# Kernel tuning notes

Measured on AMD Instinct MI355X. Metric: run time of the kernel, lower is better.

Reference implementation:

```python
import jax, jax.numpy as jnp
import numpy as np

E = 1024
H = 16          # num_heads
D = E // H      # head_dim
HID = 1024      # hidden_dim
B, S = 16, 512
EPS = 1e-5


def _ln(x, g, b):
    mu = jnp.mean(x, axis=-1, keepdims=True)
    var = jnp.mean(jnp.square(x - mu), axis=-1, keepdims=True)
    return (x - mu) * jax.lax.rsqrt(var + EPS) * g + b


def setup_inputs() -> dict:
    key = jax.random.key(0)
    ks = jax.random.split(key, 8)
    s = 1.0 / np.sqrt(E)
    return {
        'state_features': jax.random.normal(ks[0], (6, B, S, E), jnp.float32),
        'Wq': jax.random.normal(ks[1], (E, E), jnp.float32) * s,
        'bq': jnp.zeros((E,), jnp.float32),
        'Wk': jax.random.normal(ks[2], (E, E), jnp.float32) * s,
        'bk': jnp.zeros((E,), jnp.float32),
        'Wv': jax.random.normal(ks[3], (E, E), jnp.float32) * s,
        'bv': jnp.zeros((E,), jnp.float32),
        'Wo': jax.random.normal(ks[4], (E, E), jnp.float32) * s,
        'bo': jnp.zeros((E,), jnp.float32),
        'ln1_g': jnp.ones((E,), jnp.float32),
        'ln1_b': jnp.zeros((E,), jnp.float32),
        'fusion_w': jnp.ones((6,), jnp.float32) / 6.0,
        'Wf': jax.random.normal(ks[5], (HID, E), jnp.float32) * s,
        'bf': jnp.zeros((HID,), jnp.float32),
        'ln2_g': jnp.ones((HID,), jnp.float32),
        'ln2_b': jnp.zeros((HID,), jnp.float32),
    }


def reference(state_features, Wq, bq, Wk, bk, Wv, bv, Wo, bo,
              ln1_g, ln1_b, fusion_w, Wf, bf, ln2_g, ln2_b):
    # state_features: (6, B, S, E) -> stacked (N, 6, E), N = B*S
    st = jnp.transpose(state_features, (1, 2, 0, 3)).reshape(B * S, 6, E)
    N = st.shape[0]

    q = (st @ Wq.T + bq).reshape(N, 6, H, D)
    k = (st @ Wk.T + bk).reshape(N, 6, H, D)
    v = (st @ Wv.T + bv).reshape(N, 6, H, D)

    # tiny 6x6 attention per token per head (dropout = identity in eval)
    scores = jnp.einsum('nqhd,nkhd->nhqk', q, k) / np.sqrt(D).astype(np.float32)
    attn = jax.nn.softmax(scores, axis=-1)
    ctx = jnp.einsum('nhqk,nkhd->nqhd', attn, v).reshape(N, 6, E)

    out = ctx @ Wo.T + bo
    enhanced = _ln(out + st, ln1_g, ln1_b)  # (N, 6, E)

    # weighted_sum fusion
    w = jax.nn.softmax(fusion_w)
    fused = jnp.einsum('nse,s->ne', enhanced, w)

    hidden = fused @ Wf.T + bf
    hidden = jnp.where(hidden >= 0, hidden, 0.01 * hidden)  # LeakyReLU(0.01)
    hidden = _ln(hidden, ln2_g, ln2_b)
    return hidden.reshape(B, S, HID)
```

## Files before the change

### kernel.cpp

```cpp
#include <hip/hip_runtime.h>
#include <hip/hip_bf16.h>

#define NTOK 8192
#define E 1024
#define NS 6
#define MBIG (NTOK * NS)
#define NSE ((long)NTOK * E)

typedef short short8 __attribute__((ext_vector_type(8)));
typedef float f32x4 __attribute__((ext_vector_type(4)));
typedef unsigned short ushort4v __attribute__((ext_vector_type(4)));

#define TM 128
#define TN 128
#define BK 64

static __device__ __forceinline__ float bf2f(unsigned short u) {
    union { unsigned int i; float f; } c; c.i = ((unsigned int)u) << 16; return c.f;
}

struct WPtrs { const float* s[5]; __hip_bfloat16* d[5]; };
__global__ __launch_bounds__(256) void cvt5_w(WPtrs p)
{
    const int seg = blockIdx.x >> 10;
    const int i = ((blockIdx.x & 1023) * 256 + threadIdx.x) * 4;
    const float4 v = *(const float4*)(p.s[seg] + i);
    union { __hip_bfloat16 h[4]; unsigned long long u; } pk;
    pk.h[0] = (__hip_bfloat16)v.x;
    pk.h[1] = (__hip_bfloat16)v.y;
    pk.h[2] = (__hip_bfloat16)v.z;
    pk.h[3] = (__hip_bfloat16)v.w;
    *(unsigned long long*)(p.d[seg] + i) = pk.u;
}

__global__ __launch_bounds__(256) void cvt_bulk(
    const float* __restrict__ src, __hip_bfloat16* __restrict__ dst)
{
    const long i = ((long)blockIdx.x * 256 + threadIdx.x) * 4;
    const float4 v = *(const float4*)(src + i);
    union { __hip_bfloat16 h[4]; unsigned long long u; } pk;
    pk.h[0] = (__hip_bfloat16)v.x;
    pk.h[1] = (__hip_bfloat16)v.y;
    pk.h[2] = (__hip_bfloat16)v.z;
    pk.h[3] = (__hip_bfloat16)v.w;
    *(unsigned long long*)(dst + i) = pk.u;
}

#define NITER  8

struct GOut { __hip_bfloat16* C[3]; const float* bias[3]; };

static __device__ __forceinline__ void stage_half(
    const __hip_bfloat16* gsrc,
    __hip_bfloat16* ldst, int tid)
{
#pragma unroll
    for (int piece = 0; piece < 2; ++piece) {
        const int r  = piece * 64 + (tid >> 3);
        const int s  = tid & 7;
        const int ss = s ^ (r & 7);
        const __hip_bfloat16* g = gsrc + (long)r * 1024 + ss * 8;
        __hip_bfloat16* l = ldst + r * 64 + s * 8;
        __builtin_amdgcn_global_load_lds((const __attribute__((address_space(1))) void*)g,
                                         (__attribute__((address_space(3))) void*)l, 16, 0, 0);
    }
}

static __device__ __forceinline__ short8 ld_frag(
    const __hip_bfloat16* half_base, int lr, int slot)
{
    return *(const short8*)(half_base + lr * 64 + ((slot ^ (lr & 7)) << 3));
}

#define STAGE(kt, part)                                                         \
  {                                                                             \
    const int _b  = (kt) & 1;                                                   \
    const int _ab = (part) >> 1;                                                \
    const int _hf = (part) & 1;                                                 \
    const __hip_bfloat16* _g = (_ab == 0)                                       \
        ? A  + (m0 + _hf * 128) * 1024 + (kt) * 64                              \
        : Wb + ((long)n0 + _hf * 128) * 1024 + (kt) * 64;                       \
    stage_half(_g, &lds[((_b * 2 + _ab) * 2 + _hf) * 8192], tid);               \
  }

#define PH(kt, q, HASNEXT, nkt, STMT_STAGE, STMT_WAIT)                          \
  {                                                                             \
    STMT_STAGE;                                                                 \
    STMT_WAIT;                                                                  \
    __builtin_amdgcn_s_barrier();                                               \
    asm volatile("s_waitcnt lgkmcnt(0)" ::: "memory");                          \
    __builtin_amdgcn_sched_barrier(0);                                          \
    __builtin_amdgcn_s_setprio(1);                                              \
    _Pragma("unroll") for (int mf = 0; mf < 2; ++mf)                            \
      _Pragma("unroll") for (int nf = 0; nf < 4; ++nf)                          \
        _Pragma("unroll") for (int k2 = 0; k2 < 2; ++k2)                        \
          acc[(q) * 2 + mf][nf] = __builtin_amdgcn_mfma_f32_16x16x32_bf16(      \
              bfr[nf][k2], afr[(q) & 1][mf][k2], acc[(q) * 2 + mf][nf], 0,0,0); \
    __builtin_amdgcn_s_setprio(0);                                              \
    if ((q) < 3) {                                                              \
      const __hip_bfloat16* _Ab = &lds[((((kt) & 1) * 2 + 0) * 2 + wm) * 8192]; \
      _Pragma("unroll") for (int mf = 0; mf < 2; ++mf)                          \
        _Pragma("unroll") for (int k2 = 0; k2 < 2; ++k2)                        \
          afr[((q) + 1) & 1][mf][k2] =                                          \
              ld_frag(_Ab, ((q) + 1) * 32 + mf * 16 + mrow, k2 * 4 + quad);     \
    } else if (HASNEXT) {                                                       \
      const __hip_bfloat16* _An = &lds[((((nkt) & 1) * 2 + 0) * 2 + wm) * 8192];\
      const __hip_bfloat16* _Bn =                                               \
          &lds[((((nkt) & 1) * 2 + 1) * 2 + (wn >> 1)) * 8192];                 \
      _Pragma("unroll") for (int nf = 0; nf < 4; ++nf)                          \
        _Pragma("unroll") for (int k2 = 0; k2 < 2; ++k2)                        \
          bfr[nf][k2] = ld_frag(_Bn, (wn & 1) * 64 + nf * 16 + mrow,            \
                                k2 * 4 + quad);                                 \
      _Pragma("unroll") for (int mf = 0; mf < 2; ++mf)                          \
        _Pragma("unroll") for (int k2 = 0; k2 < 2; ++k2)                        \
          afr[0][mf][k2] = ld_frag(_An, mf * 16 + mrow, k2 * 4 + quad);         \
    }                                                                           \
    __builtin_amdgcn_s_barrier();                                               \
  }

__global__ __launch_bounds__(512) void gemm256(
    const __hip_bfloat16* __restrict__ A,
    const __hip_bfloat16* __restrict__ Wb,
    GOut out)
{
    __shared__ __hip_bfloat16 lds[2 * 2 * 2 * 8192] __attribute__((aligned(16)));

    const int tid  = threadIdx.x;
    const int lane = tid & 63;
    const int wid  = tid >> 6;
    const int quad = lane >> 4;
    const int mrow = lane & 15;
    const int wm = wid >> 2;
    const int wn = wid & 3;

    const int gx  = gridDim.x;
    const int nwg = gx * gridDim.y;
    const int cpx = nwg >> 3;
    const int lin = blockIdx.y * gx + blockIdx.x;
    const int tile = (lin & 7) * cpx + (lin >> 3);
    const int  n0 = (tile % gx) * 256;
    const long m0 = (long)(tile / gx) * 256;

    f32x4 acc[8][4] = {};
    short8 bfr[4][2];
    short8 afr[2][2][2];

    STAGE(0, 0); STAGE(0, 1); STAGE(0, 2); STAGE(0, 3);
    STAGE(1, 2); STAGE(1, 3);
    asm volatile("s_waitcnt vmcnt(4)" ::: "memory");
    __builtin_amdgcn_s_barrier();

    {
        const __hip_bfloat16* _Ab = &lds[(0 * 2 + wm) * 8192];
        const __hip_bfloat16* _Bb = &lds[((0 * 2 + 1) * 2 + (wn >> 1)) * 8192];
#pragma unroll
        for (int nf = 0; nf < 4; ++nf)
#pragma unroll
            for (int k2 = 0; k2 < 2; ++k2)
                bfr[nf][k2] = ld_frag(_Bb, (wn & 1) * 64 + nf * 16 + mrow, k2 * 4 + quad);
#pragma unroll
        for (int mf = 0; mf < 2; ++mf)
#pragma unroll
            for (int k2 = 0; k2 < 2; ++k2)
                afr[0][mf][k2] = ld_frag(_Ab, mf * 16 + mrow, k2 * 4 + quad);
    }

#pragma unroll 1
    for (int it = 0; it < NITER; ++it) {
        const int kt0 = 2 * it;
        const int kt1 = 2 * it + 1;
        const bool more = (it < NITER - 1);

        PH(kt0, 0, true, kt0, STAGE(kt1, 0), ((void)0));
        PH(kt0, 1, true, kt0, STAGE(kt1, 1), ((void)0));
        PH(kt0, 2, true, kt0, if (more) STAGE(kt0 + 2, 2), ((void)0));
        PH(kt0, 3, true, kt1, if (more) STAGE(kt0 + 2, 3),
           if (more) { asm volatile("s_waitcnt vmcnt(4)" ::: "memory"); }
           else      { asm volatile("s_waitcnt vmcnt(0)" ::: "memory"); });
        PH(kt1, 0, true, kt1, if (more) STAGE(kt0 + 2, 0), ((void)0));
        PH(kt1, 1, true, kt1, if (more) STAGE(kt0 + 2, 1), ((void)0));
        PH(kt1, 2, true, kt1, if (more) STAGE(kt0 + 3, 2), ((void)0));
        PH(kt1, 3, more, kt0 + 2, if (more) STAGE(kt0 + 3, 3),
           if (more) { asm volatile("s_waitcnt vmcnt(4)" ::: "memory"); });
    }

    const int seg = n0 >> 10;
    const int nb  = n0 & 1023;
    __hip_bfloat16* Cp = out.C[seg];
    const float* bp = out.bias[seg];
#pragma unroll
    for (int mf = 0; mf < 8; ++mf) {
        const long row = m0 + wm * 128 + mf * 16 + mrow;
#pragma unroll
        for (int nf = 0; nf < 4; ++nf) {
            const int colb = nb + wn * 64 + nf * 16 + quad * 4;
            const f32x4 bv4 = *(const f32x4*)(bp + colb);
            union { __hip_bfloat16 h[4]; unsigned long long u; } pk;
#pragma unroll
            for (int r = 0; r < 4; ++r)
                pk.h[r] = (__hip_bfloat16)(acc[mf][nf][r] + bv4[r]);
            *(unsigned long long*)(Cp + row * 1024 + colb) = pk.u;
        }
    }
}

__global__ __launch_bounds__(256) void gemm_bt(
    const __hip_bfloat16* __restrict__ A,
    const __hip_bfloat16* __restrict__ Wb,
    const float* __restrict__ bias,
    __hip_bfloat16* __restrict__ C)
{
    __shared__ __hip_bfloat16 lA[TM * BK] __attribute__((aligned(16)));
    __shared__ __hip_bfloat16 lB[TN * BK] __attribute__((aligned(16)));

    const int tid  = threadIdx.x;
    const int wave = tid >> 6;
    const int lane = tid & 63;
    const int quad = lane >> 4;
    const int mrow = lane & 15;
    const int wr = wave >> 1;
    const int wc = wave & 1;

    const int Gy   = gridDim.y;
    const int lin  = blockIdx.y * 8 + blockIdx.x;
    const int tile = (lin & 7) * Gy + (lin >> 3);
    const int  n0 = (tile & 7) * TN;
    const long m0 = (long)(tile >> 3) * TM;

    const int srow = lane >> 3;
    const int scol = (lane & 7) * 8;

    f32x4 acc[4][4] = {};

    for (int k0 = 0; k0 < 1024; k0 += BK) {
        __syncthreads();
#pragma unroll
        for (int it = 0; it < 4; ++it) {
            const int chunk = it * 4 + wave;
            const int row   = chunk * 8 + srow;
            const __hip_bfloat16* ga = A + (m0 + row) * 1024 + k0 + scol;
            const __hip_bfloat16* gb = Wb + (long)(n0 + row) * 1024 + k0 + scol;
            __hip_bfloat16* la = lA + row * BK + scol;
            __hip_bfloat16* lb = lB + row * BK + scol;
            __builtin_amdgcn_global_load_lds((const __attribute__((address_space(1))) void*)ga,
                                             (__attribute__((address_space(3))) void*)la, 16, 0, 0);
            __builtin_amdgcn_global_load_lds((const __attribute__((address_space(1))) void*)gb,
                                             (__attribute__((address_space(3))) void*)lb, 16, 0, 0);
        }
        __syncthreads();

#pragma unroll
        for (int kk = 0; kk < BK; kk += 32) {
            short8 af[4], bfrg[4];
#pragma unroll
            for (int i = 0; i < 4; ++i)
                af[i] = *(const short8*)(lA + (wr * 64 + i * 16 + mrow) * BK + kk + quad * 8);
#pragma unroll
            for (int j = 0; j < 4; ++j)
                bfrg[j] = *(const short8*)(lB + (wc * 64 + j * 16 + mrow) * BK + kk + quad * 8);
#pragma unroll
            for (int i = 0; i < 4; ++i)
#pragma unroll
                for (int j = 0; j < 4; ++j)
                    acc[i][j] = __builtin_amdgcn_mfma_f32_16x16x32_bf16(af[i], bfrg[j], acc[i][j], 0, 0, 0);
        }
    }

#pragma unroll
    for (int i = 0; i < 4; ++i) {
#pragma unroll
        for (int j = 0; j < 4; ++j) {
            const int col = n0 + wc * 64 + j * 16 + mrow;
            const float bv = bias[col];
#pragma unroll
            for (int r = 0; r < 4; ++r) {
                const long row = m0 + wr * 64 + i * 16 + quad * 4 + r;
                C[row * 1024 + col] = (__hip_bfloat16)(acc[i][j][r] + bv);
            }
        }
    }
}

__global__ __launch_bounds__(256) void gemm_a32_bt(
    const float* __restrict__ A,
    const __hip_bfloat16* __restrict__ Wb,
    const float* __restrict__ bias,
    __hip_bfloat16* __restrict__ C)
{
    __shared__ __hip_bfloat16 lA[TM * BK] __attribute__((aligned(16)));
    __shared__ __hip_bfloat16 lB[TN * BK] __attribute__((aligned(16)));

    const int tid  = threadIdx.x;
    const int wave = tid >> 6;
    const int lane = tid & 63;
    const int quad = lane >> 4;
    const int mrow = lane & 15;
    const int wr = wave >> 1;
    const int wc = wave & 1;

    const int Gy   = gridDim.y;
    const int lin  = blockIdx.y * 8 + blockIdx.x;
    const int tile = (lin & 7) * Gy + (lin >> 3);
    const int  n0 = (tile & 7) * TN;
    const long m0 = (long)(tile >> 3) * TM;

    const int srow = lane >> 3;
    const int scol = (lane & 7) * 8;

    f32x4 acc[4][4] = {};

    for (int k0 = 0; k0 < 1024; k0 += BK) {
        __syncthreads();
#pragma unroll
        for (int it = 0; it < 4; ++it) {
            const int chunk = it * 4 + wave;
            const int row   = chunk * 8 + srow;
            const __hip_bfloat16* gb = Wb + (long)(n0 + row) * 1024 + k0 + scol;
            __hip_bfloat16* lb = lB + row * BK + scol;
            __builtin_amdgcn_global_load_lds((const __attribute__((address_space(1))) void*)gb,
                                             (__attribute__((address_space(3))) void*)lb, 16, 0, 0);
        }
#pragma unroll
        for (int u = 0; u < 8; ++u) {
            const int c   = u * 256 + tid;
            const int row = c >> 4;
            const int c4  = c & 15;
            const float4 av = *(const float4*)(A + (m0 + row) * 1024 + k0 + c4 * 4);
            union { __hip_bfloat16 h[4]; unsigned long long uu; } pk;
            pk.h[0] = (__hip_bfloat16)av.x;
            pk.h[1] = (__hip_bfloat16)av.y;
            pk.h[2] = (__hip_bfloat16)av.z;
            pk.h[3] = (__hip_bfloat16)av.w;
            *(unsigned long long*)(lA + row * BK + c4 * 4) = pk.uu;
        }
        __syncthreads();

#pragma unroll
        for (int kk = 0; kk < BK; kk += 32) {
            short8 af[4], bfrg[4];
#pragma unroll
            for (int i = 0; i < 4; ++i)
                af[i] = *(const short8*)(lA + (wr * 64 + i * 16 + mrow) * BK + kk + quad * 8);
#pragma unroll
            for (int j = 0; j < 4; ++j)
                bfrg[j] = *(const short8*)(lB + (wc * 64 + j * 16 + mrow) * BK + kk + quad * 8);
#pragma unroll
            for (int i = 0; i < 4; ++i)
#pragma unroll
                for (int j = 0; j < 4; ++j)
                    acc[i][j] = __builtin_amdgcn_mfma_f32_16x16x32_bf16(af[i], bfrg[j], acc[i][j], 0, 0, 0);
        }
    }

#pragma unroll
    for (int i = 0; i < 4; ++i) {
#pragma unroll
        for (int j = 0; j < 4; ++j) {
            const int col = n0 + wc * 64 + j * 16 + mrow;
            const float bv = bias[col];
#pragma unroll
            for (int r = 0; r < 4; ++r) {
                const long row = m0 + wr * 64 + i * 16 + quad * 4 + r;
                C[row * 1024 + col] = (__hip_bfloat16)(acc[i][j][r] + bv);
            }
        }
    }
}

__global__ __launch_bounds__(256) void attn6(
    const __hip_bfloat16* qb,
    const __hip_bfloat16* __restrict__ kb,
    const __hip_bfloat16* __restrict__ vb,
    __hip_bfloat16* ctx)
{
    const int w    = blockIdx.x * 4 + (threadIdx.x >> 6);
    const int lane = threadIdx.x & 63;
    const int n  = w >> 2;
    const int hg = w & 3;
    const int h  = hg * 4 + (lane >> 4);
    const int sub = lane & 15;
    const long base = (long)n * 1024 + h * 64 + sub * 4;

    float qf[NS][4], kf[NS][4], vf[NS][4];
#pragma unroll
    for (int s = 0; s < NS; ++s) {
        const ushort4v qs = *(const ushort4v*)(qb + s * NSE + base);
        const ushort4v ks = *(const ushort4v*)(kb + s * NSE + base);
        const ushort4v vs = *(const ushort4v*)(vb + s * NSE + base);
#pragma unroll
        for (int c = 0; c < 4; ++c) {
            qf[s][c] = bf2f(qs[c]);
            kf[s][c] = bf2f(ks[c]);
            vf[s][c] = bf2f(vs[c]);
        }
    }

    float p[NS][NS];
#pragma unroll
    for (int i = 0; i < NS; ++i)
#pragma unroll
        for (int j = 0; j < NS; ++j) {
            float t = qf[i][0] * kf[j][0];
            t = fmaf(qf[i][1], kf[j][1], t);
            t = fmaf(qf[i][2], kf[j][2], t);
            t = fmaf(qf[i][3], kf[j][3], t);
            t += __shfl_xor(t, 1, 64);
            t += __shfl_xor(t, 2, 64);
            t += __shfl_xor(t, 4, 64);
            t += __shfl_xor(t, 8, 64);
            p[i][j] = t * 0.125f;
        }

#pragma unroll
    for (int i = 0; i < NS; ++i) {
        float m = p[i][0];
#pragma unroll
        for (int j = 1; j < NS; ++j) m = fmaxf(m, p[i][j]);
        float sum = 0.f;
#pragma unroll
        for (int j = 0; j < NS; ++j) { p[i][j] = __expf(p[i][j] - m); sum += p[i][j]; }
        const float inv = 1.0f / sum;
        float a[4] = {0.f, 0.f, 0.f, 0.f};
#pragma unroll
        for (int j = 0; j < NS; ++j)
#pragma unroll
            for (int c = 0; c < 4; ++c) a[c] = fmaf(p[i][j], vf[j][c], a[c]);
        union { __hip_bfloat16 h4[4]; unsigned long long u; } pk;
#pragma unroll
        for (int c = 0; c < 4; ++c) pk.h4[c] = (__hip_bfloat16)(a[c] * inv);
        *(unsigned long long*)(ctx + i * NSE + base) = pk.u;
    }
}

__global__ __launch_bounds__(256) void ln1_fuse(
    const __hip_bfloat16* __restrict__ wo_out,
    const float* __restrict__ sf,
    const float* __restrict__ g,
    const float* __restrict__ b,
    const float* __restrict__ fw,
    __hip_bfloat16* __restrict__ fused)
{
    const int n = blockIdx.x, tid = threadIdx.x;
    const int wave = tid >> 6, lane = tid & 63;
    const int e0 = tid * 4;

    float w[NS];
    float mx = -1e30f;
#pragma unroll
    for (int s = 0; s < NS; ++s) { w[s] = fw[s]; mx = fmaxf(mx, w[s]); }
    float sw = 0.f;
#pragma unroll
    for (int s = 0; s < NS; ++s) { w[s] = __expf(w[s] - mx); sw += w[s]; }
    const float isw = 1.0f / sw;

    const f32x4 gv4 = *(const f32x4*)(g + e0);
    const f32x4 bv4 = *(const f32x4*)(b + e0);

    __shared__ float red[2][4];
    float accf[4] = {0.f, 0.f, 0.f, 0.f};

    for (int s = 0; s < NS; ++s) {
        const long base = s * NSE + (long)n * 1024 + e0;
        const ushort4v wv = *(const ushort4v*)(wo_out + base);
        const f32x4   sv = *(const f32x4*)(sf + base);
        float x[4];
        float sum = 0.f, sq = 0.f;
#pragma unroll
        for (int c = 0; c < 4; ++c) {
            x[c] = bf2f(wv[c]) + sv[c];
            sum += x[c];
            sq  += x[c] * x[c];
        }
#pragma unroll
        for (int off = 32; off; off >>= 1) {
            sum += __shfl_xor(sum, off, 64);
            sq  += __shfl_xor(sq,  off, 64);
        }
        if (lane == 0) { red[0][wave] = sum; red[1][wave] = sq; }
        __syncthreads();
        sum = red[0][0] + red[0][1] + red[0][2] + red[0][3];
        sq  = red[1][0] + red[1][1] + red[1][2] + red[1][3];
        __syncthreads();
        const float mu   = sum * (1.0f / 1024.0f);
        const float var  = sq * (1.0f / 1024.0f) - mu * mu;
        const float rstd = rsqrtf(var + 1e-5f);
        const float ws_  = w[s] * isw;
#pragma unroll
        for (int c = 0; c < 4; ++c)
            accf[c] += ws_ * ((x[c] - mu) * rstd * gv4[c] + bv4[c]);
    }
    union { __hip_bfloat16 h4[4]; unsigned long long u; } pk;
#pragma unroll
    for (int c = 0; c < 4; ++c) pk.h4[c] = (__hip_bfloat16)accf[c];
    *(unsigned long long*)(fused + (long)n * 1024 + e0) = pk.u;
}

__global__ __launch_bounds__(256) void ln2_out(
    const __hip_bfloat16* __restrict__ hidden,
    const float* __restrict__ g,
    const float* __restrict__ b,
    float* __restrict__ out)
{
    const int n = blockIdx.x, tid = threadIdx.x;
    const int wave = tid >> 6, lane = tid & 63;
    const int e0 = tid * 4;
    __shared__ float red[2][4];

    const ushort4v hv = *(const ushort4v*)(hidden + (long)n * 1024 + e0);
    float x[4];
    float sum = 0.f, sq = 0.f;
#pragma unroll
    for (int c = 0; c < 4; ++c) {
        float t = bf2f(hv[c]);
        t = t >= 0.f ? t : 0.01f * t;
        x[c] = t;
        sum += t;
        sq  += t * t;
    }
#pragma unroll
    for (int off = 32; off; off >>= 1) {
        sum += __shfl_xor(sum, off, 64);
        sq  += __shfl_xor(sq,  off, 64);
    }
    if (lane == 0) { red[0][wave] = sum; red[1][wave] = sq; }
    __syncthreads();
    sum = red[0][0] + red[0][1] + red[0][2] + red[0][3];
    sq  = red[1][0] + red[1][1] + red[1][2] + red[1][3];
    const float mu   = sum * (1.0f / 1024.0f);
    const float var  = sq * (1.0f / 1024.0f) - mu * mu;
    const float rstd = rsqrtf(var + 1e-5f);

    const f32x4 gv4 = *(const f32x4*)(g + e0);
    const f32x4 bv4 = *(const f32x4*)(b + e0);
    f32x4 o;
#pragma unroll
    for (int c = 0; c < 4; ++c)
        o[c] = (x[c] - mu) * rstd * gv4[c] + bv4[c];
    *(f32x4*)(out + (long)n * 1024 + e0) = o;
}

extern "C" void kernel_launch(void* const* d_in, const int* in_sizes, int n_in,
                              void* d_out, int out_size, void* d_ws, size_t ws_size,
                              hipStream_t stream)
{
    const float* SF  = (const float*)d_in[0];
    const float* Wq  = (const float*)d_in[1];
    const float* bq  = (const float*)d_in[2];
    const float* Wk  = (const float*)d_in[3];
    const float* bk  = (const float*)d_in[4];
    const float* Wv  = (const float*)d_in[5];
    const float* bv  = (const float*)d_in[6];
    const float* Wo  = (const float*)d_in[7];
    const float* bo  = (const float*)d_in[8];
    const float* g1  = (const float*)d_in[9];
    const float* b1  = (const float*)d_in[10];
    const float* fw  = (const float*)d_in[11];
    const float* Wf  = (const float*)d_in[12];
    const float* bf_ = (const float*)d_in[13];
    const float* g2  = (const float*)d_in[14];
    const float* b2  = (const float*)d_in[15];
    float* out = (float*)d_out;

    const size_t REG = (size_t)MBIG * 1024 * sizeof(__hip_bfloat16);
    const size_t WTS = (size_t)5 * 1024 * 1024 * sizeof(__hip_bfloat16);
    const bool big_ws = ws_size >= 4 * REG + WTS;

    __hip_bfloat16* r0  = (__hip_bfloat16*)d_ws;
    __hip_bfloat16* r1  = r0 + (long)MBIG * 1024;
    __hip_bfloat16* r2  = r1 + (long)MBIG * 1024;
    __hip_bfloat16* r3  = r2 + (long)MBIG * 1024;
    __hip_bfloat16* wb  = big_ws ? (r3 + (long)MBIG * 1024) : r3;
    __hip_bfloat16* Wqb = wb;
    __hip_bfloat16* Wkb = Wqb + 1024 * 1024;
    __hip_bfloat16* Wvb = Wkb + 1024 * 1024;
    __hip_bfloat16* Wob = Wvb + 1024 * 1024;
    __hip_bfloat16* Wfb = Wob + 1024 * 1024;

    const dim3 blk(256);

    WPtrs wp;
    wp.s[0] = Wq; wp.s[1] = Wk; wp.s[2] = Wv; wp.s[3] = Wo; wp.s[4] = Wf;
    wp.d[0] = Wqb; wp.d[1] = Wkb; wp.d[2] = Wvb; wp.d[3] = Wob; wp.d[4] = Wfb;
    cvt5_w<<<5 * 1024, blk, 0, stream>>>(wp);

    cvt_bulk<<<MBIG, blk, 0, stream>>>(SF, r2);

    if (big_ws) {
        const dim3 blk2(512);
        const dim3 gQKV(12, MBIG / 256);
        const dim3 gB2(4, MBIG / 256);
        const dim3 gSm2(4, NTOK / 256);

        GOut oqkv;
        oqkv.C[0] = r0; oqkv.C[1] = r1; oqkv.C[2] = r3;
        oqkv.bias[0] = bq; oqkv.bias[1] = bk; oqkv.bias[2] = bv;
        gemm256<<<gQKV, blk2, 0, stream>>>(r2, Wqb, oqkv);

        attn6<<<NTOK, blk, 0, stream>>>(r0, r1, r3, r0);

        GOut owo;
        owo.C[0] = r1; owo.C[1] = r1; owo.C[2] = r1;
        owo.bias[0] = bo; owo.bias[1] = bo; owo.bias[2] = bo;
        gemm256<<<gB2, blk2, 0, stream>>>(r0, Wob, owo);

        ln1_fuse<<<NTOK, blk, 0, stream>>>(r1, SF, g1, b1, fw, r2);

        GOut owf;
        owf.C[0] = r0; owf.C[1] = r0; owf.C[2] = r0;
        owf.bias[0] = bf_; owf.bias[1] = bf_; owf.bias[2] = bf_;
        gemm256<<<gSm2, blk2, 0, stream>>>(r2, Wfb, owf);

        ln2_out<<<NTOK, blk, 0, stream>>>(r0, g2, b2, out);
    } else {
        const dim3 gBig(8, MBIG / TM);
        const dim3 gSm(8, NTOK / TM);

        gemm_bt<<<gBig, blk, 0, stream>>>(r2, Wqb, bq, r0);
        gemm_bt<<<gBig, blk, 0, stream>>>(r2, Wkb, bk, r1);
        gemm_a32_bt<<<gBig, blk, 0, stream>>>(SF, Wvb, bv, r2);
        attn6<<<NTOK, blk, 0, stream>>>(r0, r1, r2, r0);
        gemm_bt<<<gBig, blk, 0, stream>>>(r0, Wob, bo, r1);
        ln1_fuse<<<NTOK, blk, 0, stream>>>(r1, SF, g1, b1, fw, r2);
        gemm_bt<<<gSm, blk, 0, stream>>>(r2, Wfb, bf_, r0);
        ln2_out<<<NTOK, blk, 0, stream>>>(r0, g2, b2, out);
    }
}
```

Before: 928.5 us.

## Restructure GEMM main loop into two-quarter sections and use 128-tile GEMM for final projection

```diff
diff --git a/kernel.cpp b/kernel.cpp
--- a/kernel.cpp
+++ b/kernel.cpp
@@ -83,38 +83,62 @@
     stage_half(_g, &lds[((_b * 2 + _ab) * 2 + _hf) * 8192], tid);               \
   }
 
-#define PH(kt, q, HASNEXT, nkt, STMT_STAGE, STMT_WAIT)                          \
+#define POST_A(kt, q)                                                           \
+  {                                                                             \
+    const __hip_bfloat16* _Ab = &lds[((((kt) & 1) * 2 + 0) * 2 + wm) * 8192];   \
+    _Pragma("unroll") for (int mf = 0; mf < 2; ++mf)                            \
+      _Pragma("unroll") for (int k2 = 0; k2 < 2; ++k2)                          \
+        afr[0][mf][k2] = ld_frag(_Ab, (q) * 32 + mf * 16 + mrow, k2 * 4 + quad);\
+  }
+
+#define POST_NEXT(nkt)                                                          \
+  {                                                                             \
+    const __hip_bfloat16* _An = &lds[((((nkt) & 1) * 2 + 0) * 2 + wm) * 8192];  \
+    const __hip_bfloat16* _Bn =                                                 \
+        &lds[((((nkt) & 1) * 2 + 1) * 2 + (wn >> 1)) * 8192];                   \
+    _Pragma("unroll") for (int nf = 0; nf < 4; ++nf)                            \
+      _Pragma("unroll") for (int k2 = 0; k2 < 2; ++k2)                          \
+        bfr[nf][k2] = ld_frag(_Bn, (wn & 1) * 64 + nf * 16 + mrow,              \
+                              k2 * 4 + quad);                                   \
+    _Pragma("unroll") for (int mf = 0; mf < 2; ++mf)                            \
+      _Pragma("unroll") for (int k2 = 0; k2 < 2; ++k2)                          \
+        afr[0][mf][k2] = ld_frag(_An, mf * 16 + mrow, k2 * 4 + quad);           \
+  }
+
+#define SEC(kt, qlo, STMT_STAGE, STMT_WAIT, STMT_POST)                          \
   {                                                                             \
     STMT_STAGE;                                                                 \
     STMT_WAIT;                                                                  \
     __builtin_amdgcn_s_barrier();                                               \
     asm volatile("s_waitcnt lgkmcnt(0)" ::: "memory");                          \
     __builtin_amdgcn_sched_barrier(0);                                          \
+    {                                                                           \
+      const __hip_bfloat16* _Ab = &lds[((((kt) & 1) * 2 + 0) * 2 + wm) * 8192]; \
+      _Pragma("unroll") for (int mf = 0; mf < 2; ++mf)                          \
+        _Pragma("unroll") for (int k2 = 0; k2 < 2; ++k2)                        \
+          afr[1][mf][k2] = ld_frag(_Ab, ((qlo) + 1) * 32 + mf * 16 + mrow,      \
+                                   k2 * 4 + quad);                              \
+    }                                                                           \
+    __builtin_amdgcn_sched_barrier(0);                                          \
     __builtin_amdgcn_s_setprio(1);                                              \
     _Pragma("unroll") for (int mf = 0; mf < 2; ++mf)                            \
       _Pragma("unroll") for (int nf = 0; nf < 4; ++nf)                          \
         _Pragma("unroll") for (int k2 = 0; k2 < 2; ++k2)                        \
-          acc[(q) * 2 + mf][nf] = __builtin_amdgcn_mfma_f32_16x16x32_bf16(      \
-              bfr[nf][k2], afr[(q) & 1][mf][k2], acc[(q) * 2 + mf][nf], 0,0,0); \
+          acc[(qlo) * 2 + mf][nf] = __builtin_amdgcn_mfma_f32_16x16x32_bf16(    \
+              bfr[nf][k2], afr[0][mf][k2], acc[(qlo) * 2 + mf][nf], 0, 0, 0);   \
     __builtin_amdgcn_s_setprio(0);                                              \
-    if ((q) < 3) {                                                              \
-      const __hip_bfloat16* _Ab = &lds[((((kt) & 1) * 2 + 0) * 2 + wm) * 8192]; \
-      _Pragma("unroll") for (int mf = 0; mf < 2; ++mf)                          \
-        _Pragma("unroll") for (int k2 = 0; k2 < 2; ++k2)                        \
-          afr[((q) + 1) & 1][mf][k2] =                                          \
-              ld_frag(_Ab, ((q) + 1) * 32 + mf * 16 + mrow, k2 * 4 + quad);     \
-    } else if (HASNEXT) {                                                       \
-      const __hip_bfloat16* _An = &lds[((((nkt) & 1) * 2 + 0) * 2 + wm) * 8192];\
-      const __hip_bfloat16* _Bn =                                               \
-          &lds[((((nkt) & 1) * 2 + 1) * 2 + (wn >> 1)) * 8192];                 \
+    asm volatile("s_waitcnt lgkmcnt(0)" ::: "memory");                          \
+    __builtin_amdgcn_sched_barrier(0);                                          \
+    __builtin_amdgcn_s_setprio(1);                                              \
+    _Pragma("unroll") for (int mf = 0; mf < 2; ++mf)                            \
       _Pragma("unroll") for (int nf = 0; nf < 4; ++nf)                          \
         _Pragma("unroll") for (int k2 = 0; k2 < 2; ++k2)                        \
-          bfr[nf][k2] = ld_frag(_Bn, (wn & 1) * 64 + nf * 16 + mrow,            \
-                                k2 * 4 + quad);                                 \
-      _Pragma("unroll") for (int mf = 0; mf < 2; ++mf)                          \
-        _Pragma("unroll") for (int k2 = 0; k2 < 2; ++k2)                        \
-          afr[0][mf][k2] = ld_frag(_An, mf * 16 + mrow, k2 * 4 + quad);         \
-    }                                                                           \
+          acc[((qlo) + 1) * 2 + mf][nf] =                                       \
+              __builtin_amdgcn_mfma_f32_16x16x32_bf16(                          \
+                  bfr[nf][k2], afr[1][mf][k2],                                  \
+                  acc[((qlo) + 1) * 2 + mf][nf], 0, 0, 0);                      \
+    __builtin_amdgcn_s_setprio(0);                                              \
+    STMT_POST;                                                                  \
     __builtin_amdgcn_s_barrier();                                               \
   }
 
@@ -171,17 +195,17 @@
         const int kt1 = 2 * it + 1;
         const bool more = (it < NITER - 1);
 
-        PH(kt0, 0, true, kt0, STAGE(kt1, 0), ((void)0));
-        PH(kt0, 1, true, kt0, STAGE(kt1, 1), ((void)0));
-        PH(kt0, 2, true, kt0, if (more) STAGE(kt0 + 2, 2), ((void)0));
-        PH(kt0, 3, true, kt1, if (more) STAGE(kt0 + 2, 3),
-           if (more) { asm volatile("s_waitcnt vmcnt(4)" ::: "memory"); }
-           else      { asm volatile("s_waitcnt vmcnt(0)" ::: "memory"); });
-        PH(kt1, 0, true, kt1, if (more) STAGE(kt0 + 2, 0), ((void)0));
-        PH(kt1, 1, true, kt1, if (more) STAGE(kt0 + 2, 1), ((void)0));
-        PH(kt1, 2, true, kt1, if (more) STAGE(kt0 + 3, 2), ((void)0));
-        PH(kt1, 3, more, kt0 + 2, if (more) STAGE(kt0 + 3, 3),
-           if (more) { asm volatile("s_waitcnt vmcnt(4)" ::: "memory"); });
+        SEC(kt0, 0, { STAGE(kt1, 0); STAGE(kt1, 1); }, ((void)0),
+            POST_A(kt0, 2));
+        SEC(kt0, 2, if (more) { STAGE(kt0 + 2, 2); STAGE(kt0 + 2, 3); },
+            if (more) { asm volatile("s_waitcnt vmcnt(4)" ::: "memory"); }
+            else      { asm volatile("s_waitcnt vmcnt(0)" ::: "memory"); },
+            POST_NEXT(kt1));
+        SEC(kt1, 0, if (more) { STAGE(kt0 + 2, 0); STAGE(kt0 + 2, 1); }, ((void)0),
+            POST_A(kt1, 2));
+        SEC(kt1, 2, if (more) { STAGE(kt0 + 3, 2); STAGE(kt0 + 3, 3); },
+            if (more) { asm volatile("s_waitcnt vmcnt(4)" ::: "memory"); },
+            if (more) POST_NEXT(kt0 + 2));
     }
 
     const int seg = n0 >> 10;
@@ -589,7 +613,6 @@
         const dim3 blk2(512);
         const dim3 gQKV(12, MBIG / 256);
         const dim3 gB2(4, MBIG / 256);
-        const dim3 gSm2(4, NTOK / 256);
 
         GOut oqkv;
         oqkv.C[0] = r0; oqkv.C[1] = r1; oqkv.C[2] = r3;
@@ -605,10 +628,7 @@
 
         ln1_fuse<<<NTOK, blk, 0, stream>>>(r1, SF, g1, b1, fw, r2);
 
-        GOut owf;
-        owf.C[0] = r0; owf.C[1] = r0; owf.C[2] = r0;
-        owf.bias[0] = bf_; owf.bias[1] = bf_; owf.bias[2] = bf_;
-        gemm256<<<gSm2, blk2, 0, stream>>>(r2, Wfb, owf);
+        gemm_bt<<<dim3(8, NTOK / TM), blk, 0, stream>>>(r2, Wfb, bf_, r0);
 
         ln2_out<<<NTOK, blk, 0, stream>>>(r0, g2, b2, out);
     } else {
```

After: 950.5 us. 2.4% more time.
